# Optimization experiments

Measured on AMD Instinct MI355X. Metric: run time of the kernel, lower is better.

Reference implementation:

```python
import jax, jax.numpy as jnp
import numpy as np

KEY_DIM = 512
VALUE_DIM = 128
CAPACITY = 500000
N_RETRIEVE = 32
LN_EPS = 1e-5       # torch nn.LayerNorm default
NORM_EPS = 1e-12    # torch F.normalize default


def setup_inputs() -> dict:
    key = jax.random.key(0)
    ks = jax.random.split(key, 5)
    w_scale = 0.02
    return {
        "query": jax.random.normal(ks[0], (1, KEY_DIM), dtype=jnp.float32),
        "W1": jax.random.normal(ks[1], (KEY_DIM, KEY_DIM), dtype=jnp.float32) * w_scale,
        "b1": jnp.zeros((KEY_DIM,), dtype=jnp.float32),
        "W2": jax.random.normal(ks[2], (KEY_DIM, KEY_DIM), dtype=jnp.float32) * w_scale,
        "b2": jnp.zeros((KEY_DIM,), dtype=jnp.float32),
        "ln_g": jnp.ones((KEY_DIM,), dtype=jnp.float32),
        "ln_b": jnp.zeros((KEY_DIM,), dtype=jnp.float32),
        "keys": jax.random.normal(ks[3], (CAPACITY, KEY_DIM), dtype=jnp.float32),
        "values": jax.random.normal(ks[4], (CAPACITY, VALUE_DIM), dtype=jnp.float32),
    }


def _l2_normalize(x, axis=-1):
    # matches torch F.normalize: x / max(||x||, eps)
    n = jnp.linalg.norm(x, axis=axis, keepdims=True)
    return x / jnp.maximum(n, NORM_EPS)


def _layer_norm(x, g, b):
    mu = jnp.mean(x, axis=-1, keepdims=True)
    var = jnp.mean(jnp.square(x - mu), axis=-1, keepdims=True)
    return (x - mu) * jax.lax.rsqrt(var + LN_EPS) * g + b


def reference(query, W1, b1, W2, b2, ln_g, ln_b, keys, values):
    # EpisodicMemory.read_aggregated with a full memory bank (n == capacity).
    q_in = jax.lax.stop_gradient(query)                 # query.detach()
    h = jax.nn.silu(q_in @ W1.T + b1) @ W2.T + b2       # key_proj MLP, [1, K]
    h = _layer_norm(h, ln_g, ln_b)                      # key_norm
    q = _l2_normalize(h)[0]                             # [K]
    kn = _l2_normalize(keys)                            # [C, K]
    sim = kn @ q                                        # cosine sims, [C]
    top_sim, top_idx = jax.lax.top_k(sim, N_RETRIEVE)   # [k], [k]
    vals = values[top_idx]                              # gather, [k, V]
    attn = jax.nn.softmax(top_sim, axis=0)              # [k]
    return jnp.sum(vals * attn[:, None], axis=0)        # [V]
```

## Files before the change

### kernel.cpp

```cpp
#include <hip/hip_runtime.h>
#include <math.h>

#define KEY_DIM   512
#define VALUE_DIM 128
#define CAP       500000
#define NRET      32
#define LN_EPS    1e-5f
#define NORM_EPS  1e-12f
#define NEG_INF   (-3.402823466e38f)
#define IDX_INF   0x7fffffff

#define SCAN_BLOCKS 489
#define NCAND       (SCAN_BLOCKS * 4 * 32)
#define M1_BLOCKS   62
#define N2          (M1_BLOCKS * 32)


template<int CTRL>
__device__ inline float dppMovF(float x) {
  return __int_as_float(__builtin_amdgcn_update_dpp(0, __float_as_int(x), CTRL, 0xF, 0xF, true));
}

__device__ inline float waveSumF(float x) {
  x += dppMovF<0xB1>(x);
  x += dppMovF<0x4E>(x);
  x += dppMovF<0x124>(x);
  x += dppMovF<0x128>(x);
  x += __int_as_float(__builtin_amdgcn_ds_swizzle(__float_as_int(x), 0x401F));
  x += __shfl_xor(x, 32);
  return x;
}

template<int D>
__device__ inline int fetchI(int x) {
  if constexpr (D == 1)       return __builtin_amdgcn_update_dpp(0, x, 0xB1, 0xF, 0xF, true);
  else if constexpr (D == 2)  return __builtin_amdgcn_update_dpp(0, x, 0x4E, 0xF, 0xF, true);
  else if constexpr (D == 4)  return __builtin_amdgcn_ds_swizzle(x, 0x101F);
  else if constexpr (D == 8)  return __builtin_amdgcn_ds_swizzle(x, 0x201F);
  else if constexpr (D == 16) return __builtin_amdgcn_ds_swizzle(x, 0x401F);
  else                        return __shfl_xor(x, 32);
}
template<int D>
__device__ inline float fetchF(float x) { return __int_as_float(fetchI<D>(__float_as_int(x))); }

template<int D>
__device__ inline void amStep(float& v, int& g, int& c) {
  float ov = fetchF<D>(v); int og = fetchI<D>(g); int oc = fetchI<D>(c);
  if (ov > v || (ov == v && og < g)) { v = ov; g = og; c = oc; }
}
__device__ inline void waveArgMax3(float& v, int& g, int& c) {
  amStep<1>(v, g, c); amStep<2>(v, g, c); amStep<4>(v, g, c);
  amStep<8>(v, g, c); amStep<16>(v, g, c); amStep<32>(v, g, c);
}

template<int D>
__device__ inline void ceStageLane(float& v, int& gi, bool desc, int lane) {
  float ov = fetchF<D>(v); int og = fetchI<D>(gi);
  bool better  = (ov > v) || (ov == v && og < gi);
  bool amLower = (lane & D) == 0;
  bool keepMax = (amLower == desc);
  if (keepMax == better) { v = ov; gi = og; }
}

__device__ inline void ceStageReg(float& vA, int& gA, float& vB, int& gB, bool desc) {
  bool better = (vB > vA) || (vB == vA && gB < gA);
  bool sw = (better == desc);
  float tv = sw ? vB : vA; vB = sw ? vA : vB; vA = tv;
  int   tg = sw ? gB : gA; gB = sw ? gA : gB; gA = tg;
}


__global__ __launch_bounds__(256) void matvec1_kernel(
    const float* __restrict__ query, const float* __restrict__ W1,
    const float* __restrict__ b1, float* __restrict__ h)
{
  int tid = threadIdx.x, wid = tid >> 6, lane = tid & 63;
  int row = (blockIdx.x << 2) + wid;
  const float4* q4 = (const float4*)query;
  const float4* wrow = (const float4*)(W1 + (size_t)row * KEY_DIM);
  float4 a0 = wrow[lane],      q0 = q4[lane];
  float4 a1 = wrow[lane + 64], q1 = q4[lane + 64];
  float acc = a0.x*q0.x + a0.y*q0.y + a0.z*q0.z + a0.w*q0.w
            + a1.x*q1.x + a1.y*q1.y + a1.z*q1.z + a1.w*q1.w;
  acc = waveSumF(acc);
  if (lane == 0) {
    float x = acc + b1[row];
    h[row] = x / (1.f + expf(-x));
  }
}

__global__ __launch_bounds__(256) void matvec2_kernel(
    const float* __restrict__ h, const float* __restrict__ W2,
    const float* __restrict__ b2, float* __restrict__ g)
{
  int tid = threadIdx.x, wid = tid >> 6, lane = tid & 63;
  int row = (blockIdx.x << 2) + wid;
  const float4* h4 = (const float4*)h;
  const float4* wrow = (const float4*)(W2 + (size_t)row * KEY_DIM);
  float4 a0 = wrow[lane],      q0 = h4[lane];
  float4 a1 = wrow[lane + 64], q1 = h4[lane + 64];
  float acc = a0.x*q0.x + a0.y*q0.y + a0.z*q0.z + a0.w*q0.w
            + a1.x*q1.x + a1.y*q1.y + a1.z*q1.z + a1.w*q1.w;
  acc = waveSumF(acc);
  if (lane == 0) g[row] = acc + b2[row];
}


__global__ __launch_bounds__(256, 4) void scan_kernel(
    const float* __restrict__ keys, const float* __restrict__ g,
    const float* __restrict__ ln_g, const float* __restrict__ ln_b,
    float* __restrict__ cand_val, int* __restrict__ cand_idx)
{
  const int tid = threadIdx.x, wid = tid >> 6, lane = tid & 63;

  const float4* g4 = (const float4*)g;
  float4 x0 = g4[lane], x1 = g4[lane + 64];
  float psum = x0.x + x0.y + x0.z + x0.w + x1.x + x1.y + x1.z + x1.w;
  float mu = waveSumF(psum) * (1.f / 512.f);
  float4 d0, d1;
  d0.x = x0.x - mu; d0.y = x0.y - mu; d0.z = x0.z - mu; d0.w = x0.w - mu;
  d1.x = x1.x - mu; d1.y = x1.y - mu; d1.z = x1.z - mu; d1.w = x1.w - mu;
  float pvar = d0.x*d0.x + d0.y*d0.y + d0.z*d0.z + d0.w*d0.w
             + d1.x*d1.x + d1.y*d1.y + d1.z*d1.z + d1.w*d1.w;
  float var  = waveSumF(pvar) * (1.f / 512.f);
  float rstd = 1.f / sqrtf(var + LN_EPS);
  const float4* lg4 = (const float4*)ln_g;
  const float4* lb4 = (const float4*)ln_b;
  float4 a0 = lg4[lane], a1 = lg4[lane + 64];
  float4 b0 = lb4[lane], b1 = lb4[lane + 64];
  float4 y0, y1;
  y0.x = d0.x*rstd*a0.x + b0.x; y0.y = d0.y*rstd*a0.y + b0.y;
  y0.z = d0.z*rstd*a0.z + b0.z; y0.w = d0.w*rstd*a0.w + b0.w;
  y1.x = d1.x*rstd*a1.x + b1.x; y1.y = d1.y*rstd*a1.y + b1.y;
  y1.z = d1.z*rstd*a1.z + b1.z; y1.w = d1.w*rstd*a1.w + b1.w;
  float pn  = y0.x*y0.x + y0.y*y0.y + y0.z*y0.z + y0.w*y0.w
            + y1.x*y1.x + y1.y*y1.y + y1.z*y1.z + y1.w*y1.w;
  float nsq = waveSumF(pn);
  float nf  = 1.f / fmaxf(sqrtf(nsq), NORM_EPS);
  float4 q0, q1;
  q0.x = y0.x*nf; q0.y = y0.y*nf; q0.z = y0.z*nf; q0.w = y0.w*nf;
  q1.x = y1.x*nf; q1.y = y1.y*nf; q1.z = y1.z*nf; q1.w = y1.w*nf;

  const char* kl = (const char*)keys + (size_t)lane * 16;
  const int wrow0 = (blockIdx.x << 10) + (wid << 8);

  float sv[4]; int sg[4];

  #pragma unroll
  for (int seg = 0; seg < 4; ++seg) {
    const int segbase = wrow0 + (seg << 6);
    float simreg = NEG_INF;
    #pragma unroll 1
    for (int bi = 0; bi < 8; ++bi) {
      const int r0 = segbase + (bi << 3);
      float4 A[8], B[8];
      #pragma unroll
      for (int i = 0; i < 8; ++i) {
        int rr = min(r0 + i, CAP - 1);
        const char* rp = kl + (size_t)rr * 2048;
        A[i] = *(const float4*)rp;
        B[i] = *(const float4*)(rp + 1024);
      }
      float dt[8], sq[8];
      #pragma unroll
      for (int i = 0; i < 8; ++i) {
        dt[i] = A[i].x*q0.x + A[i].y*q0.y + A[i].z*q0.z + A[i].w*q0.w
              + B[i].x*q1.x + B[i].y*q1.y + B[i].z*q1.z + B[i].w*q1.w;
        sq[i] = A[i].x*A[i].x + A[i].y*A[i].y + A[i].z*A[i].z + A[i].w*A[i].w
              + B[i].x*B[i].x + B[i].y*B[i].y + B[i].z*B[i].z + B[i].w*B[i].w;
      }
      #pragma unroll
      for (int i = 0; i < 8; ++i) { dt[i] = waveSumF(dt[i]); sq[i] = waveSumF(sq[i]); }
      #pragma unroll
      for (int i = 0; i < 8; ++i) {
        float sim = dt[i] / fmaxf(sqrtf(sq[i]), NORM_EPS);
        bool ok = (r0 + i) < CAP;
        sim = ok ? sim : NEG_INF;
        int rb = (bi << 3) + i;
        simreg = (lane == rb) ? sim : simreg;
      }
    }
    sv[seg] = simreg;
    sg[seg] = segbase + lane;
  }

  #define LST4(D, A0, A1, A2, A3) \
    ceStageLane<D>(sv[0], sg[0], A0, lane); \
    ceStageLane<D>(sv[1], sg[1], A1, lane); \
    ceStageLane<D>(sv[2], sg[2], A2, lane); \
    ceStageLane<D>(sv[3], sg[3], A3, lane);

  { bool dm = (lane & 2) == 0;  LST4(1, dm,dm,dm,dm) }
  { bool dm = (lane & 4) == 0;  LST4(2, dm,dm,dm,dm)  LST4(1, dm,dm,dm,dm) }
  { bool dm = (lane & 8) == 0;  LST4(4, dm,dm,dm,dm)  LST4(2, dm,dm,dm,dm)
                                LST4(1, dm,dm,dm,dm) }
  { bool dm = (lane & 16) == 0; LST4(8, dm,dm,dm,dm)  LST4(4, dm,dm,dm,dm)
                                LST4(2, dm,dm,dm,dm)  LST4(1, dm,dm,dm,dm) }
  { bool dm = (lane & 32) == 0; LST4(16, dm,dm,dm,dm) LST4(8, dm,dm,dm,dm)
                                LST4(4, dm,dm,dm,dm)  LST4(2, dm,dm,dm,dm)
                                LST4(1, dm,dm,dm,dm) }
  LST4(32, true,false,true,false) LST4(16, true,false,true,false)
  LST4(8,  true,false,true,false) LST4(4,  true,false,true,false)
  LST4(2,  true,false,true,false) LST4(1,  true,false,true,false)
  ceStageReg(sv[0], sg[0], sv[1], sg[1], true);
  ceStageReg(sv[2], sg[2], sv[3], sg[3], false);
  LST4(32, true,true,false,false) LST4(16, true,true,false,false)
  LST4(8,  true,true,false,false) LST4(4,  true,true,false,false)
  LST4(2,  true,true,false,false) LST4(1,  true,true,false,false)
  ceStageReg(sv[0], sg[0], sv[2], sg[2], true);
  ceStageReg(sv[1], sg[1], sv[3], sg[3], true);
  ceStageReg(sv[0], sg[0], sv[1], sg[1], true);
  ceStageReg(sv[2], sg[2], sv[3], sg[3], true);
  LST4(32, true,true,true,true) LST4(16, true,true,true,true)
  LST4(8,  true,true,true,true) LST4(4,  true,true,true,true)
  LST4(2,  true,true,true,true) LST4(1,  true,true,true,true)
  #undef LST4

  if (lane < NRET) {
    int w = (blockIdx.x << 2) + wid;
    cand_val[w * NRET + lane] = sv[0];
    cand_idx[w * NRET + lane] = sg[0];
  }
}


__global__ __launch_bounds__(256) void merge_kernel(
    const float* __restrict__ in_val, const int* __restrict__ in_idx, int n,
    float* __restrict__ out_val, int* __restrict__ out_idx)
{
  __shared__ float lv[128];
  __shared__ int   li[128];
  int tid = threadIdx.x, wid = tid >> 6, lane = tid & 63;

  float vs[4]; int gs[4];
  int base = (blockIdx.x << 10) + (wid << 8);
  #pragma unroll
  for (int k = 0; k < 4; ++k) {
    int idx = base + (k << 6) + lane;
    bool ok = idx < n;
    vs[k] = ok ? in_val[idx] : NEG_INF;
    gs[k] = ok ? in_idx[idx] : IDX_INF;
  }
  for (int it = 0; it < NRET; ++it) {
    float bv = vs[0]; int bg = gs[0]; int bs = 0;
    #pragma unroll
    for (int k = 1; k < 4; ++k)
      if (vs[k] > bv || (vs[k] == bv && gs[k] < bg)) { bv = vs[k]; bg = gs[k]; bs = k; }
    int code = (lane << 2) | bs;
    waveArgMax3(bv, bg, code);
    if (lane == (code >> 2)) {
      int s = code & 3;
      if (s == 0) vs[0] = NEG_INF; else if (s == 1) vs[1] = NEG_INF;
      else if (s == 2) vs[2] = NEG_INF; else vs[3] = NEG_INF;
    }
    if (lane == 0) { lv[(wid << 5) + it] = bv; li[(wid << 5) + it] = bg; }
  }
  __syncthreads();
  if (wid == 0) {
    float c0 = lv[lane], c1 = lv[64 + lane];
    int   h0 = li[lane], h1 = li[64 + lane];
    for (int it = 0; it < NRET; ++it) {
      bool p1 = (c1 > c0) || (c1 == c0 && h1 < h0);
      float bv = p1 ? c1 : c0; int bg = p1 ? h1 : h0;
      int code = (lane << 1) | (p1 ? 1 : 0);
      waveArgMax3(bv, bg, code);
      if (lane == (code >> 1)) { if (code & 1) c1 = NEG_INF; else c0 = NEG_INF; }
      if (lane == 0) {
        out_val[(blockIdx.x << 5) + it] = bv;
        out_idx[(blockIdx.x << 5) + it] = bg;
      }
    }
  }
}


__global__ __launch_bounds__(256) void final_kernel(
    const float* __restrict__ c2v, const int* __restrict__ c2i, int n,
    const float* __restrict__ values, float* __restrict__ out)
{
  __shared__ float lv[128];
  __shared__ int   li[128];
  __shared__ float selv[NRET];
  __shared__ int   seli[NRET];
  __shared__ float attn[NRET];
  int tid = threadIdx.x, wid = tid >> 6, lane = tid & 63;

  float vs[8]; int gs[8];
  int base = (wid << 9);
  #pragma unroll
  for (int k = 0; k < 8; ++k) {
    int idx = base + (k << 6) + lane;
    bool ok = idx < n;
    vs[k] = ok ? c2v[idx] : NEG_INF;
    gs[k] = ok ? c2i[idx] : IDX_INF;
  }
  for (int it = 0; it < NRET; ++it) {
    float bv = vs[0]; int bg = gs[0]; int bs = 0;
    #pragma unroll
    for (int k = 1; k < 8; ++k)
      if (vs[k] > bv || (vs[k] == bv && gs[k] < bg)) { bv = vs[k]; bg = gs[k]; bs = k; }
    int code = (lane << 3) | bs;
    waveArgMax3(bv, bg, code);
    if (lane == (code >> 3)) {
      int s = code & 7;
      #pragma unroll
      for (int k = 0; k < 8; ++k) if (k == s) vs[k] = NEG_INF;
    }
    if (lane == 0) { lv[(wid << 5) + it] = bv; li[(wid << 5) + it] = bg; }
  }
  __syncthreads();
  if (wid == 0) {
    float c0 = lv[lane], c1 = lv[64 + lane];
    int   h0 = li[lane], h1 = li[64 + lane];
    for (int it = 0; it < NRET; ++it) {
      bool p1 = (c1 > c0) || (c1 == c0 && h1 < h0);
      float bv = p1 ? c1 : c0; int bg = p1 ? h1 : h0;
      int code = (lane << 1) | (p1 ? 1 : 0);
      waveArgMax3(bv, bg, code);
      if (lane == (code >> 1)) { if (code & 1) c1 = NEG_INF; else c0 = NEG_INF; }
      if (lane == 0) { selv[it] = bv; seli[it] = bg; }
    }
  }
  __syncthreads();
  if (tid < NRET) {
    float e = expf(selv[tid] - selv[0]);
    float s = e;
    #pragma unroll
    for (int off = 16; off; off >>= 1) s += __shfl_xor(s, off);
    attn[tid] = e / s;
  }
  __syncthreads();
  if (tid < VALUE_DIM) {
    float acc = 0.f;
    #pragma unroll
    for (int k = 0; k < NRET; ++k)
      acc += attn[k] * values[(size_t)seli[k] * VALUE_DIM + tid];
    out[tid] = acc;
  }
}


extern "C" void kernel_launch(void* const* d_in, const int* in_sizes, int n_in,
                              void* d_out, int out_size, void* d_ws, size_t ws_size,
                              hipStream_t stream) {
  const float* query  = (const float*)d_in[0];
  const float* W1     = (const float*)d_in[1];
  const float* b1     = (const float*)d_in[2];
  const float* W2     = (const float*)d_in[3];
  const float* b2     = (const float*)d_in[4];
  const float* ln_g   = (const float*)d_in[5];
  const float* ln_b   = (const float*)d_in[6];
  const float* keys   = (const float*)d_in[7];
  const float* values = (const float*)d_in[8];
  float* out = (float*)d_out;

  float* wsf = (float*)d_ws;
  float* h        = wsf;
  float* g        = wsf + 512;
  float* cand_val = wsf + 1024;
  int*   cand_idx = (int*)(wsf + 1024 + NCAND);
  float* c2v      = wsf + 1024 + 2 * NCAND;
  int*   c2i      = (int*)(wsf + 1024 + 2 * NCAND + N2);

  hipLaunchKernelGGL(matvec1_kernel, dim3(128), dim3(256), 0, stream, query, W1, b1, h);
  hipLaunchKernelGGL(matvec2_kernel, dim3(128), dim3(256), 0, stream, h, W2, b2, g);
  hipLaunchKernelGGL(scan_kernel, dim3(SCAN_BLOCKS), dim3(256), 0, stream,
                     keys, g, ln_g, ln_b, cand_val, cand_idx);
  hipLaunchKernelGGL(merge_kernel, dim3(M1_BLOCKS), dim3(256), 0, stream,
                     cand_val, cand_idx, NCAND, c2v, c2i);
  hipLaunchKernelGGL(final_kernel, dim3(1), dim3(256), 0, stream,
                     c2v, c2i, N2, values, out);
}
```

Measured before the change: 278.8 us.

## Restructure key scan to 16-lane rows with double-buffered loads; fuse block merge

The scan kernel now gives each row to a 16-lane group, so one wave handles four rows at once and reduces with DPP row sums only. Key rows are double-buffered in registers so the next loads are issued while the current rows are reduced. The LayerNorm query is computed once per block into shared memory. Each block now merges its waves' top-32 itself, which removes the separate merge kernel, and a 1024-thread final kernel takes the larger candidate list. This cuts wave-level reductions and one launch, at the cost of more registers and a heavier single-block final selection.

After: 353.1 us. 1.27x slower.

```diff
diff --git a/kernel.cpp b/kernel.cpp
--- a/kernel.cpp
+++ b/kernel.cpp
@@ -10,10 +10,11 @@
 #define NEG_INF   (-3.402823466e38f)
 #define IDX_INF   0x7fffffff
 
-#define SCAN_BLOCKS 489
-#define NCAND       (SCAN_BLOCKS * 4 * 32)
-#define M1_BLOCKS   62
-#define N2          (M1_BLOCKS * 32)
+#define ROWS_PER_WAVE  128
+#define ROWS_PER_BLOCK 512
+#define SCAN_BLOCKS    977
+#define NCAND          (SCAN_BLOCKS * NRET)
+#define FIN_SLOTS      31
 
 
 template<int CTRL>
@@ -21,11 +22,16 @@
   return __int_as_float(__builtin_amdgcn_update_dpp(0, __float_as_int(x), CTRL, 0xF, 0xF, true));
 }
 
-__device__ inline float waveSumF(float x) {
+__device__ inline float rowSum16(float x) {
   x += dppMovF<0xB1>(x);
   x += dppMovF<0x4E>(x);
   x += dppMovF<0x124>(x);
   x += dppMovF<0x128>(x);
+  return x;
+}
+
+__device__ inline float waveSumF(float x) {
+  x = rowSum16(x);
   x += __int_as_float(__builtin_amdgcn_ds_swizzle(__float_as_int(x), 0x401F));
   x += __shfl_xor(x, 32);
   return x;
@@ -111,150 +117,115 @@
     const float* __restrict__ ln_g, const float* __restrict__ ln_b,
     float* __restrict__ cand_val, int* __restrict__ cand_idx)
 {
-  const int tid = threadIdx.x, wid = tid >> 6, lane = tid & 63;
-
-  const float4* g4 = (const float4*)g;
-  float4 x0 = g4[lane], x1 = g4[lane + 64];
-  float psum = x0.x + x0.y + x0.z + x0.w + x1.x + x1.y + x1.z + x1.w;
-  float mu = waveSumF(psum) * (1.f / 512.f);
-  float4 d0, d1;
-  d0.x = x0.x - mu; d0.y = x0.y - mu; d0.z = x0.z - mu; d0.w = x0.w - mu;
-  d1.x = x1.x - mu; d1.y = x1.y - mu; d1.z = x1.z - mu; d1.w = x1.w - mu;
-  float pvar = d0.x*d0.x + d0.y*d0.y + d0.z*d0.z + d0.w*d0.w
-             + d1.x*d1.x + d1.y*d1.y + d1.z*d1.z + d1.w*d1.w;
-  float var  = waveSumF(pvar) * (1.f / 512.f);
-  float rstd = 1.f / sqrtf(var + LN_EPS);
-  const float4* lg4 = (const float4*)ln_g;
-  const float4* lb4 = (const float4*)ln_b;
-  float4 a0 = lg4[lane], a1 = lg4[lane + 64];
-  float4 b0 = lb4[lane], b1 = lb4[lane + 64];
-  float4 y0, y1;
-  y0.x = d0.x*rstd*a0.x + b0.x; y0.y = d0.y*rstd*a0.y + b0.y;
-  y0.z = d0.z*rstd*a0.z + b0.z; y0.w = d0.w*rstd*a0.w + b0.w;
-  y1.x = d1.x*rstd*a1.x + b1.x; y1.y = d1.y*rstd*a1.y + b1.y;
-  y1.z = d1.z*rstd*a1.z + b1.z; y1.w = d1.w*rstd*a1.w + b1.w;
-  float pn  = y0.x*y0.x + y0.y*y0.y + y0.z*y0.z + y0.w*y0.w
-            + y1.x*y1.x + y1.y*y1.y + y1.z*y1.z + y1.w*y1.w;
-  float nsq = waveSumF(pn);
-  float nf  = 1.f / fmaxf(sqrtf(nsq), NORM_EPS);
-  float4 q0, q1;
-  q0.x = y0.x*nf; q0.y = y0.y*nf; q0.z = y0.z*nf; q0.w = y0.w*nf;
-  q1.x = y1.x*nf; q1.y = y1.y*nf; q1.z = y1.z*nf; q1.w = y1.w*nf;
-
-  const char* kl = (const char*)keys + (size_t)lane * 16;
-  const int wrow0 = (blockIdx.x << 10) + (wid << 8);
-
-  float sv[4]; int sg[4];
-
-  #pragma unroll
-  for (int seg = 0; seg < 4; ++seg) {
-    const int segbase = wrow0 + (seg << 6);
-    float simreg = NEG_INF;
-    #pragma unroll 1
-    for (int bi = 0; bi < 8; ++bi) {
-      const int r0 = segbase + (bi << 3);
-      float4 A[8], B[8];
-      #pragma unroll
-      for (int i = 0; i < 8; ++i) {
-        int rr = min(r0 + i, CAP - 1);
-        const char* rp = kl + (size_t)rr * 2048;
-        A[i] = *(const float4*)rp;
-        B[i] = *(const float4*)(rp + 1024);
-      }
-      float dt[8], sq[8];
-      #pragma unroll
-      for (int i = 0; i < 8; ++i) {
-        dt[i] = A[i].x*q0.x + A[i].y*q0.y + A[i].z*q0.z + A[i].w*q0.w
-              + B[i].x*q1.x + B[i].y*q1.y + B[i].z*q1.z + B[i].w*q1.w;
-        sq[i] = A[i].x*A[i].x + A[i].y*A[i].y + A[i].z*A[i].z + A[i].w*A[i].w
-              + B[i].x*B[i].x + B[i].y*B[i].y + B[i].z*B[i].z + B[i].w*B[i].w;
-      }
-      #pragma unroll
-      for (int i = 0; i < 8; ++i) { dt[i] = waveSumF(dt[i]); sq[i] = waveSumF(sq[i]); }
-      #pragma unroll
-      for (int i = 0; i < 8; ++i) {
-        float sim = dt[i] / fmaxf(sqrtf(sq[i]), NORM_EPS);
-        bool ok = (r0 + i) < CAP;
-        sim = ok ? sim : NEG_INF;
-        int rb = (bi << 3) + i;
-        simreg = (lane == rb) ? sim : simreg;
-      }
-    }
-    sv[seg] = simreg;
-    sg[seg] = segbase + lane;
-  }
-
-  #define LST4(D, A0, A1, A2, A3) \
-    ceStageLane<D>(sv[0], sg[0], A0, lane); \
-    ceStageLane<D>(sv[1], sg[1], A1, lane); \
-    ceStageLane<D>(sv[2], sg[2], A2, lane); \
-    ceStageLane<D>(sv[3], sg[3], A3, lane);
-
-  { bool dm = (lane & 2) == 0;  LST4(1, dm,dm,dm,dm) }
-  { bool dm = (lane & 4) == 0;  LST4(2, dm,dm,dm,dm)  LST4(1, dm,dm,dm,dm) }
-  { bool dm = (lane & 8) == 0;  LST4(4, dm,dm,dm,dm)  LST4(2, dm,dm,dm,dm)
-                                LST4(1, dm,dm,dm,dm) }
-  { bool dm = (lane & 16) == 0; LST4(8, dm,dm,dm,dm)  LST4(4, dm,dm,dm,dm)
-                                LST4(2, dm,dm,dm,dm)  LST4(1, dm,dm,dm,dm) }
-  { bool dm = (lane & 32) == 0; LST4(16, dm,dm,dm,dm) LST4(8, dm,dm,dm,dm)
-                                LST4(4, dm,dm,dm,dm)  LST4(2, dm,dm,dm,dm)
-                                LST4(1, dm,dm,dm,dm) }
-  LST4(32, true,false,true,false) LST4(16, true,false,true,false)
-  LST4(8,  true,false,true,false) LST4(4,  true,false,true,false)
-  LST4(2,  true,false,true,false) LST4(1,  true,false,true,false)
-  ceStageReg(sv[0], sg[0], sv[1], sg[1], true);
-  ceStageReg(sv[2], sg[2], sv[3], sg[3], false);
-  LST4(32, true,true,false,false) LST4(16, true,true,false,false)
-  LST4(8,  true,true,false,false) LST4(4,  true,true,false,false)
-  LST4(2,  true,true,false,false) LST4(1,  true,true,false,false)
-  ceStageReg(sv[0], sg[0], sv[2], sg[2], true);
-  ceStageReg(sv[1], sg[1], sv[3], sg[3], true);
-  ceStageReg(sv[0], sg[0], sv[1], sg[1], true);
-  ceStageReg(sv[2], sg[2], sv[3], sg[3], true);
-  LST4(32, true,true,true,true) LST4(16, true,true,true,true)
-  LST4(8,  true,true,true,true) LST4(4,  true,true,true,true)
-  LST4(2,  true,true,true,true) LST4(1,  true,true,true,true)
-  #undef LST4
-
-  if (lane < NRET) {
-    int w = (blockIdx.x << 2) + wid;
-    cand_val[w * NRET + lane] = sv[0];
-    cand_idx[w * NRET + lane] = sg[0];
-  }
-}
-
-
-__global__ __launch_bounds__(256) void merge_kernel(
-    const float* __restrict__ in_val, const int* __restrict__ in_idx, int n,
-    float* __restrict__ out_val, int* __restrict__ out_idx)
-{
+  __shared__ float qs[512];
   __shared__ float lv[128];
   __shared__ int   li[128];
-  int tid = threadIdx.x, wid = tid >> 6, lane = tid & 63;
-
-  float vs[4]; int gs[4];
-  int base = (blockIdx.x << 10) + (wid << 8);
-  #pragma unroll
-  for (int k = 0; k < 4; ++k) {
-    int idx = base + (k << 6) + lane;
-    bool ok = idx < n;
-    vs[k] = ok ? in_val[idx] : NEG_INF;
-    gs[k] = ok ? in_idx[idx] : IDX_INF;
-  }
-  for (int it = 0; it < NRET; ++it) {
-    float bv = vs[0]; int bg = gs[0]; int bs = 0;
-    #pragma unroll
-    for (int k = 1; k < 4; ++k)
-      if (vs[k] > bv || (vs[k] == bv && gs[k] < bg)) { bv = vs[k]; bg = gs[k]; bs = k; }
-    int code = (lane << 2) | bs;
-    waveArgMax3(bv, bg, code);
-    if (lane == (code >> 2)) {
-      int s = code & 3;
-      if (s == 0) vs[0] = NEG_INF; else if (s == 1) vs[1] = NEG_INF;
-      else if (s == 2) vs[2] = NEG_INF; else vs[3] = NEG_INF;
+  const int tid = threadIdx.x, wid = tid >> 6, lane = tid & 63;
+  const int sub = lane & 15, grp = lane >> 4;
+
+  if (wid == 0) {
+    const float4* g4 = (const float4*)g;
+    float4 x0 = g4[lane], x1 = g4[lane + 64];
+    float psum = x0.x + x0.y + x0.z + x0.w + x1.x + x1.y + x1.z + x1.w;
+    float mu = waveSumF(psum) * (1.f / 512.f);
+    float4 d0, d1;
+    d0.x = x0.x - mu; d0.y = x0.y - mu; d0.z = x0.z - mu; d0.w = x0.w - mu;
+    d1.x = x1.x - mu; d1.y = x1.y - mu; d1.z = x1.z - mu; d1.w = x1.w - mu;
+    float pvar = d0.x*d0.x + d0.y*d0.y + d0.z*d0.z + d0.w*d0.w
+               + d1.x*d1.x + d1.y*d1.y + d1.z*d1.z + d1.w*d1.w;
+    float var  = waveSumF(pvar) * (1.f / 512.f);
+    float rstd = 1.f / sqrtf(var + LN_EPS);
+    const float4* lg4 = (const float4*)ln_g;
+    const float4* lb4 = (const float4*)ln_b;
+    float4 a0 = lg4[lane], a1 = lg4[lane + 64];
+    float4 b0 = lb4[lane], b1 = lb4[lane + 64];
+    float4 y0, y1;
+    y0.x = d0.x*rstd*a0.x + b0.x; y0.y = d0.y*rstd*a0.y + b0.y;
+    y0.z = d0.z*rstd*a0.z + b0.z; y0.w = d0.w*rstd*a0.w + b0.w;
+    y1.x = d1.x*rstd*a1.x + b1.x; y1.y = d1.y*rstd*a1.y + b1.y;
+    y1.z = d1.z*rstd*a1.z + b1.z; y1.w = d1.w*rstd*a1.w + b1.w;
+    float pn  = y0.x*y0.x + y0.y*y0.y + y0.z*y0.z + y0.w*y0.w
+              + y1.x*y1.x + y1.y*y1.y + y1.z*y1.z + y1.w*y1.w;
+    float nsq = waveSumF(pn);
+    float nf  = 1.f / fmaxf(sqrtf(nsq), NORM_EPS);
+    float4 q0, q1;
+    q0.x = y0.x*nf; q0.y = y0.y*nf; q0.z = y0.z*nf; q0.w = y0.w*nf;
+    q1.x = y1.x*nf; q1.y = y1.y*nf; q1.z = y1.z*nf; q1.w = y1.w*nf;
+    ((float4*)qs)[lane]      = q0;
+    ((float4*)qs)[lane + 64] = q1;
+  }
+  __syncthreads();
+
+  float4 qf[8];
+  {
+    const float4* qs4 = (const float4*)qs;
+    #pragma unroll
+    for (int k = 0; k < 8; ++k) qf[k] = qs4[(k << 4) + sub];
+  }
+
+  const int wrow0 = blockIdx.x * ROWS_PER_BLOCK + wid * ROWS_PER_WAVE;
+  const char* kbase = (const char*)keys + (size_t)sub * 16;
+
+  float4 buf[2][8];
+  float sv0 = NEG_INF, sv1 = NEG_INF;
+
+  {
+    int r = min(wrow0 + grp, CAP - 1);
+    const char* p = kbase + (size_t)r * 2048;
+    #pragma unroll
+    for (int k = 0; k < 8; ++k) buf[0][k] = *(const float4*)(p + (k << 8));
+  }
+
+  #pragma unroll 1
+  for (int jo = 0; jo < 4; ++jo) {
+    #pragma unroll
+    for (int ju = 0; ju < 8; ++ju) {
+      const int j = (jo << 3) + ju;
+      const int cur = ju & 1, nxt = cur ^ 1;
+      {
+        int rn = min(wrow0 + ((j + 1) << 2) + grp, CAP - 1);
+        const char* p = kbase + (size_t)rn * 2048;
+        #pragma unroll
+        for (int k = 0; k < 8; ++k) buf[nxt][k] = *(const float4*)(p + (k << 8));
+      }
+      float dot = 0.f, ss = 0.f;
+      #pragma unroll
+      for (int k = 0; k < 8; ++k) {
+        float4 a = buf[cur][k];
+        dot += a.x*qf[k].x + a.y*qf[k].y + a.z*qf[k].z + a.w*qf[k].w;
+        ss  += a.x*a.x + a.y*a.y + a.z*a.z + a.w*a.w;
+      }
+      dot = rowSum16(dot);
+      ss  = rowSum16(ss);
+      float sim = dot / fmaxf(sqrtf(ss), NORM_EPS);
+      int r = wrow0 + (j << 2) + grp;
+      sim = (r < CAP) ? sim : NEG_INF;
+      bool cap = (sub == (j & 15));
+      if (j < 16) { if (cap) sv0 = sim; }
+      else        { if (cap) sv1 = sim; }
     }
-    if (lane == 0) { lv[(wid << 5) + it] = bv; li[(wid << 5) + it] = bg; }
-  }
+  }
+
+  int sg0 = wrow0 + (sub << 2) + grp;
+  int sg1 = sg0 + 64;
+
+  #define LST2(D, A0, A1) \
+    ceStageLane<D>(sv0, sg0, A0, lane); \
+    ceStageLane<D>(sv1, sg1, A1, lane);
+  { bool dm = (lane & 2) == 0;  LST2(1, dm,dm) }
+  { bool dm = (lane & 4) == 0;  LST2(2, dm,dm)  LST2(1, dm,dm) }
+  { bool dm = (lane & 8) == 0;  LST2(4, dm,dm)  LST2(2, dm,dm)  LST2(1, dm,dm) }
+  { bool dm = (lane & 16) == 0; LST2(8, dm,dm)  LST2(4, dm,dm)  LST2(2, dm,dm)  LST2(1, dm,dm) }
+  { bool dm = (lane & 32) == 0; LST2(16, dm,dm) LST2(8, dm,dm)  LST2(4, dm,dm)
+                                LST2(2, dm,dm)  LST2(1, dm,dm) }
+  LST2(32, true,false) LST2(16, true,false) LST2(8, true,false)
+  LST2(4,  true,false) LST2(2,  true,false) LST2(1, true,false)
+  ceStageReg(sv0, sg0, sv1, sg1, true);
+  LST2(32, true,true) LST2(16, true,true) LST2(8, true,true)
+  LST2(4,  true,true) LST2(2,  true,true) LST2(1, true,true)
+  #undef LST2
+
+  if (lane < NRET) { lv[(wid << 5) + lane] = sv0; li[(wid << 5) + lane] = sg0; }
   __syncthreads();
   if (wid == 0) {
     float c0 = lv[lane], c1 = lv[64 + lane];
@@ -266,58 +237,64 @@
       waveArgMax3(bv, bg, code);
       if (lane == (code >> 1)) { if (code & 1) c1 = NEG_INF; else c0 = NEG_INF; }
       if (lane == 0) {
-        out_val[(blockIdx.x << 5) + it] = bv;
-        out_idx[(blockIdx.x << 5) + it] = bg;
+        cand_val[(blockIdx.x << 5) + it] = bv;
+        cand_idx[(blockIdx.x << 5) + it] = bg;
       }
     }
   }
 }
 
 
-__global__ __launch_bounds__(256) void final_kernel(
-    const float* __restrict__ c2v, const int* __restrict__ c2i, int n,
+__global__ __launch_bounds__(1024) void final_kernel(
+    const float* __restrict__ cv, const int* __restrict__ ci, int n,
     const float* __restrict__ values, float* __restrict__ out)
 {
-  __shared__ float lv[128];
-  __shared__ int   li[128];
+  __shared__ float wv[512];
+  __shared__ int   wgi[512];
   __shared__ float selv[NRET];
   __shared__ int   seli[NRET];
   __shared__ float attn[NRET];
   int tid = threadIdx.x, wid = tid >> 6, lane = tid & 63;
 
-  float vs[8]; int gs[8];
-  int base = (wid << 9);
+  float vs[FIN_SLOTS]; int gs[FIN_SLOTS];
   #pragma unroll
-  for (int k = 0; k < 8; ++k) {
-    int idx = base + (k << 6) + lane;
+  for (int k = 0; k < FIN_SLOTS; ++k) {
+    int idx = (k << 10) + tid;
     bool ok = idx < n;
-    vs[k] = ok ? c2v[idx] : NEG_INF;
-    gs[k] = ok ? c2i[idx] : IDX_INF;
+    vs[k] = ok ? cv[idx] : NEG_INF;
+    gs[k] = ok ? ci[idx] : IDX_INF;
   }
   for (int it = 0; it < NRET; ++it) {
     float bv = vs[0]; int bg = gs[0]; int bs = 0;
     #pragma unroll
-    for (int k = 1; k < 8; ++k)
+    for (int k = 1; k < FIN_SLOTS; ++k)
       if (vs[k] > bv || (vs[k] == bv && gs[k] < bg)) { bv = vs[k]; bg = gs[k]; bs = k; }
-    int code = (lane << 3) | bs;
+    int code = (lane << 5) | bs;
     waveArgMax3(bv, bg, code);
-    if (lane == (code >> 3)) {
-      int s = code & 7;
+    if (lane == (code >> 5)) {
+      int s = code & 31;
       #pragma unroll
-      for (int k = 0; k < 8; ++k) if (k == s) vs[k] = NEG_INF;
+      for (int k = 0; k < FIN_SLOTS; ++k) if (k == s) vs[k] = NEG_INF;
     }
-    if (lane == 0) { lv[(wid << 5) + it] = bv; li[(wid << 5) + it] = bg; }
+    if (lane == 0) { wv[(wid << 5) + it] = bv; wgi[(wid << 5) + it] = bg; }
   }
   __syncthreads();
   if (wid == 0) {
-    float c0 = lv[lane], c1 = lv[64 + lane];
-    int   h0 = li[lane], h1 = li[64 + lane];
+    float fs[8]; int fg[8];
+    #pragma unroll
+    for (int k = 0; k < 8; ++k) { fs[k] = wv[(k << 6) + lane]; fg[k] = wgi[(k << 6) + lane]; }
     for (int it = 0; it < NRET; ++it) {
-      bool p1 = (c1 > c0) || (c1 == c0 && h1 < h0);
-      float bv = p1 ? c1 : c0; int bg = p1 ? h1 : h0;
-      int code = (lane << 1) | (p1 ? 1 : 0);
+      float bv = fs[0]; int bg = fg[0]; int bs = 0;
+      #pragma unroll
+      for (int k = 1; k < 8; ++k)
+        if (fs[k] > bv || (fs[k] == bv && fg[k] < bg)) { bv = fs[k]; bg = fg[k]; bs = k; }
+      int code = (lane << 3) | bs;
       waveArgMax3(bv, bg, code);
-      if (lane == (code >> 1)) { if (code & 1) c1 = NEG_INF; else c0 = NEG_INF; }
+      if (lane == (code >> 3)) {
+        int s = code & 7;
+        #pragma unroll
+        for (int k = 0; k < 8; ++k) if (k == s) fs[k] = NEG_INF;
+      }
       if (lane == 0) { selv[it] = bv; seli[it] = bg; }
     }
   }
@@ -359,15 +336,11 @@
   float* g        = wsf + 512;
   float* cand_val = wsf + 1024;
   int*   cand_idx = (int*)(wsf + 1024 + NCAND);
-  float* c2v      = wsf + 1024 + 2 * NCAND;
-  int*   c2i      = (int*)(wsf + 1024 + 2 * NCAND + N2);
 
   hipLaunchKernelGGL(matvec1_kernel, dim3(128), dim3(256), 0, stream, query, W1, b1, h);
   hipLaunchKernelGGL(matvec2_kernel, dim3(128), dim3(256), 0, stream, h, W2, b2, g);
   hipLaunchKernelGGL(scan_kernel, dim3(SCAN_BLOCKS), dim3(256), 0, stream,
                      keys, g, ln_g, ln_b, cand_val, cand_idx);
-  hipLaunchKernelGGL(merge_kernel, dim3(M1_BLOCKS), dim3(256), 0, stream,
-                     cand_val, cand_idx, NCAND, c2v, c2i);
-  hipLaunchKernelGGL(final_kernel, dim3(1), dim3(256), 0, stream,
-                     c2v, c2i, N2, values, out);
-}
+  hipLaunchKernelGGL(final_kernel, dim3(1), dim3(1024), 0, stream,
+                     cand_val, cand_idx, NCAND, values, out);
+}
```

## Fold first top-k merge into scan kernel and widen final reduction block

Applied to the files above, without the earlier changes.

The scan kernel now merges its four per-wave top-32 lists in shared memory and writes one top-32 per block, which removes the separate merge kernel launch. The final kernel runs with 1024 threads and 16 slots per thread, reducing the 489*32 block candidates directly, with an 8-way per-lane merge of the 16 wave results. This saves one launch and a global round trip, but adds serial merge work at the tail of every scan block and a larger single-block final reduction.

Measured after the change: 299.7 us. 7.5% more time.

```diff
diff --git a/kernel.cpp b/kernel.cpp
--- a/kernel.cpp
+++ b/kernel.cpp
@@ -11,9 +11,8 @@
 #define IDX_INF   0x7fffffff
 
 #define SCAN_BLOCKS 489
-#define NCAND       (SCAN_BLOCKS * 4 * 32)
-#define M1_BLOCKS   62
-#define N2          (M1_BLOCKS * 32)
+#define NCAND       (SCAN_BLOCKS * NRET)
+#define FIN_SLOTS   16
 
 
 template<int CTRL>
@@ -111,6 +110,8 @@
     const float* __restrict__ ln_g, const float* __restrict__ ln_b,
     float* __restrict__ cand_val, int* __restrict__ cand_idx)
 {
+  __shared__ float lv[128];
+  __shared__ int   li[128];
   const int tid = threadIdx.x, wid = tid >> 6, lane = tid & 63;
 
   const float4* g4 = (const float4*)g;
@@ -216,45 +217,7 @@
   LST4(2,  true,true,true,true) LST4(1,  true,true,true,true)
   #undef LST4
 
-  if (lane < NRET) {
-    int w = (blockIdx.x << 2) + wid;
-    cand_val[w * NRET + lane] = sv[0];
-    cand_idx[w * NRET + lane] = sg[0];
-  }
-}
-
-
-__global__ __launch_bounds__(256) void merge_kernel(
-    const float* __restrict__ in_val, const int* __restrict__ in_idx, int n,
-    float* __restrict__ out_val, int* __restrict__ out_idx)
-{
-  __shared__ float lv[128];
-  __shared__ int   li[128];
-  int tid = threadIdx.x, wid = tid >> 6, lane = tid & 63;
-
-  float vs[4]; int gs[4];
-  int base = (blockIdx.x << 10) + (wid << 8);
-  #pragma unroll
-  for (int k = 0; k < 4; ++k) {
-    int idx = base + (k << 6) + lane;
-    bool ok = idx < n;
-    vs[k] = ok ? in_val[idx] : NEG_INF;
-    gs[k] = ok ? in_idx[idx] : IDX_INF;
-  }
-  for (int it = 0; it < NRET; ++it) {
-    float bv = vs[0]; int bg = gs[0]; int bs = 0;
-    #pragma unroll
-    for (int k = 1; k < 4; ++k)
-      if (vs[k] > bv || (vs[k] == bv && gs[k] < bg)) { bv = vs[k]; bg = gs[k]; bs = k; }
-    int code = (lane << 2) | bs;
-    waveArgMax3(bv, bg, code);
-    if (lane == (code >> 2)) {
-      int s = code & 3;
-      if (s == 0) vs[0] = NEG_INF; else if (s == 1) vs[1] = NEG_INF;
-      else if (s == 2) vs[2] = NEG_INF; else vs[3] = NEG_INF;
-    }
-    if (lane == 0) { lv[(wid << 5) + it] = bv; li[(wid << 5) + it] = bg; }
-  }
+  if (lane < NRET) { lv[(wid << 5) + lane] = sv[0]; li[(wid << 5) + lane] = sg[0]; }
   __syncthreads();
   if (wid == 0) {
     float c0 = lv[lane], c1 = lv[64 + lane];
@@ -266,58 +229,64 @@
       waveArgMax3(bv, bg, code);
       if (lane == (code >> 1)) { if (code & 1) c1 = NEG_INF; else c0 = NEG_INF; }
       if (lane == 0) {
-        out_val[(blockIdx.x << 5) + it] = bv;
-        out_idx[(blockIdx.x << 5) + it] = bg;
+        cand_val[(blockIdx.x << 5) + it] = bv;
+        cand_idx[(blockIdx.x << 5) + it] = bg;
       }
     }
   }
 }
 
 
-__global__ __launch_bounds__(256) void final_kernel(
-    const float* __restrict__ c2v, const int* __restrict__ c2i, int n,
+__global__ __launch_bounds__(1024) void final_kernel(
+    const float* __restrict__ cv, const int* __restrict__ ci, int n,
     const float* __restrict__ values, float* __restrict__ out)
 {
-  __shared__ float lv[128];
-  __shared__ int   li[128];
+  __shared__ float wv[512];
+  __shared__ int   wgi[512];
   __shared__ float selv[NRET];
   __shared__ int   seli[NRET];
   __shared__ float attn[NRET];
   int tid = threadIdx.x, wid = tid >> 6, lane = tid & 63;
 
-  float vs[8]; int gs[8];
-  int base = (wid << 9);
+  float vs[FIN_SLOTS]; int gs[FIN_SLOTS];
   #pragma unroll
-  for (int k = 0; k < 8; ++k) {
-    int idx = base + (k << 6) + lane;
+  for (int k = 0; k < FIN_SLOTS; ++k) {
+    int idx = (k << 10) + tid;
     bool ok = idx < n;
-    vs[k] = ok ? c2v[idx] : NEG_INF;
-    gs[k] = ok ? c2i[idx] : IDX_INF;
+    vs[k] = ok ? cv[idx] : NEG_INF;
+    gs[k] = ok ? ci[idx] : IDX_INF;
   }
   for (int it = 0; it < NRET; ++it) {
     float bv = vs[0]; int bg = gs[0]; int bs = 0;
     #pragma unroll
-    for (int k = 1; k < 8; ++k)
+    for (int k = 1; k < FIN_SLOTS; ++k)
       if (vs[k] > bv || (vs[k] == bv && gs[k] < bg)) { bv = vs[k]; bg = gs[k]; bs = k; }
-    int code = (lane << 3) | bs;
+    int code = (lane << 4) | bs;
     waveArgMax3(bv, bg, code);
-    if (lane == (code >> 3)) {
-      int s = code & 7;
-      #pragma unroll
-      for (int k = 0; k < 8; ++k) if (k == s) vs[k] = NEG_INF;
+    if (lane == (code >> 4)) {
+      int s = code & 15;
+      #pragma unroll
+      for (int k = 0; k < FIN_SLOTS; ++k) if (k == s) vs[k] = NEG_INF;
     }
-    if (lane == 0) { lv[(wid << 5) + it] = bv; li[(wid << 5) + it] = bg; }
+    if (lane == 0) { wv[(wid << 5) + it] = bv; wgi[(wid << 5) + it] = bg; }
   }
   __syncthreads();
   if (wid == 0) {
-    float c0 = lv[lane], c1 = lv[64 + lane];
-    int   h0 = li[lane], h1 = li[64 + lane];
+    float fs[8]; int fg[8];
+    #pragma unroll
+    for (int k = 0; k < 8; ++k) { fs[k] = wv[(k << 6) + lane]; fg[k] = wgi[(k << 6) + lane]; }
     for (int it = 0; it < NRET; ++it) {
-      bool p1 = (c1 > c0) || (c1 == c0 && h1 < h0);
-      float bv = p1 ? c1 : c0; int bg = p1 ? h1 : h0;
-      int code = (lane << 1) | (p1 ? 1 : 0);
+      float bv = fs[0]; int bg = fg[0]; int bs = 0;
+      #pragma unroll
+      for (int k = 1; k < 8; ++k)
+        if (fs[k] > bv || (fs[k] == bv && fg[k] < bg)) { bv = fs[k]; bg = fg[k]; bs = k; }
+      int code = (lane << 3) | bs;
       waveArgMax3(bv, bg, code);
-      if (lane == (code >> 1)) { if (code & 1) c1 = NEG_INF; else c0 = NEG_INF; }
+      if (lane == (code >> 3)) {
+        int s = code & 7;
+        #pragma unroll
+        for (int k = 0; k < 8; ++k) if (k == s) fs[k] = NEG_INF;
+      }
       if (lane == 0) { selv[it] = bv; seli[it] = bg; }
     }
   }
@@ -359,15 +328,11 @@
   float* g        = wsf + 512;
   float* cand_val = wsf + 1024;
   int*   cand_idx = (int*)(wsf + 1024 + NCAND);
-  float* c2v      = wsf + 1024 + 2 * NCAND;
-  int*   c2i      = (int*)(wsf + 1024 + 2 * NCAND + N2);
 
   hipLaunchKernelGGL(matvec1_kernel, dim3(128), dim3(256), 0, stream, query, W1, b1, h);
   hipLaunchKernelGGL(matvec2_kernel, dim3(128), dim3(256), 0, stream, h, W2, b2, g);
   hipLaunchKernelGGL(scan_kernel, dim3(SCAN_BLOCKS), dim3(256), 0, stream,
                      keys, g, ln_g, ln_b, cand_val, cand_idx);
-  hipLaunchKernelGGL(merge_kernel, dim3(M1_BLOCKS), dim3(256), 0, stream,
-                     cand_val, cand_idx, NCAND, c2v, c2i);
-  hipLaunchKernelGGL(final_kernel, dim3(1), dim3(256), 0, stream,
-                     c2v, c2i, N2, values, out);
-}
+  hipLaunchKernelGGL(final_kernel, dim3(1), dim3(1024), 0, stream,
+                     cand_val, cand_idx, NCAND, values, out);
+}
```
